# Kernel optimization log

Measured on AMD Instinct MI355X. Metric: run time of the kernel, lower is better.

## Reference

```python
import jax, jax.numpy as jnp
import numpy as np

N, E, B = 250000, 1000000, 500
FD = 78  # num_features_xd


def setup_inputs() -> dict:
    key = jax.random.key(0)
    ks = jax.random.split(key, 24)
    g = lambda i, shape, fan_in: jax.random.normal(ks[i], shape, jnp.float32) / np.sqrt(fan_in)
    inp = {
        "x": jax.random.normal(ks[0], (N, FD), jnp.float32),
        "edge_index": jax.random.randint(ks[1], (2, E), 0, N, jnp.int32),
        "batch": jnp.repeat(jnp.arange(B, dtype=jnp.int32), N // B),  # sorted, every graph non-empty
        "target": jax.random.randint(ks[2], (B, 1000), 0, 26, jnp.int32),
        # GCN layers
        "W1": g(3, (FD, FD), FD), "b1": jnp.zeros((FD,), jnp.float32),
        "W2": g(4, (FD, 2 * FD), FD), "b2": jnp.zeros((2 * FD,), jnp.float32),
        "W3": g(5, (2 * FD, 4 * FD), 2 * FD), "b3": jnp.zeros((4 * FD,), jnp.float32),
        # graph head
        "fcg1_w": g(6, (4 * FD, 1024), 4 * FD), "fcg1_b": jnp.zeros((1024,), jnp.float32),
        "fcg2_w": g(7, (1024, 128), 1024), "fcg2_b": jnp.zeros((128,), jnp.float32),
        # protein branch
        "emb": g(8, (26, 128), 1),
        "conv_w": g(9, (32, 1000, 8), 1000 * 8), "conv_b": jnp.zeros((32,), jnp.float32),
        "fcxt_w": g(10, (32 * 121, 128), 32 * 121), "fcxt_b": jnp.zeros((128,), jnp.float32),
        # fusion head
        "fc1_w": g(11, (256, 1024), 256), "fc1_b": jnp.zeros((1024,), jnp.float32),
        "fc2_w": g(12, (1024, 512), 1024), "fc2_b": jnp.zeros((512,), jnp.float32),
        "out_w": g(13, (512, 1), 512), "out_b": jnp.zeros((1,), jnp.float32),
    }
    return inp


def _gcn_conv(x, W, b, src, dst, dinv, n):
    # PyG GCNConv: out = D^-1/2 (A+I) D^-1/2 (x W) + b, symmetric norm with self-loops
    xw = x @ W
    norm = dinv[src] * dinv[dst]                                   # [E]
    agg = jax.ops.segment_sum(xw[src] * norm[:, None], dst, num_segments=n)
    agg = agg + xw * (dinv * dinv)[:, None]                        # self-loop term
    return agg + b


def reference(x, edge_index, batch, target,
              W1, b1, W2, b2, W3, b3,
              fcg1_w, fcg1_b, fcg2_w, fcg2_b,
              emb, conv_w, conv_b, fcxt_w, fcxt_b,
              fc1_w, fc1_b, fc2_w, fc2_b, out_w, out_b):
    n = x.shape[0]
    src, dst = edge_index[0], edge_index[1]
    # degree with self-loops (edge weights 1)
    deg = jax.ops.segment_sum(jnp.ones((src.shape[0],), x.dtype), dst, num_segments=n) + 1.0
    dinv = jax.lax.rsqrt(deg)

    h = jax.nn.relu(_gcn_conv(x, W1, b1, src, dst, dinv, n))
    h = jax.nn.relu(_gcn_conv(h, W2, b2, src, dst, dinv, n))
    h = jax.nn.relu(_gcn_conv(h, W3, b3, src, dst, dinv, n))

    bsz = fcg2_w.shape[1] * 0 + target.shape[0]  # B
    g = jax.ops.segment_max(h, batch, num_segments=bsz)            # global max pool -> [B, 312]
    g = jax.nn.relu(g @ fcg1_w + fcg1_b)
    g = g @ fcg2_w + fcg2_b                                        # dropout = identity (eval)

    # protein branch: Conv1d over embedding dim (channels = seq positions = 1000)
    e = emb[target]                                                # [B, 1000, 128]
    c = jax.lax.conv_general_dilated(e, conv_w, window_strides=(1,), padding="VALID",
                                     dimension_numbers=("NCH", "OIH", "NCH"))
    c = c + conv_b[None, :, None]                                  # [B, 32, 121]
    xt = c.reshape(bsz, 32 * 121) @ fcxt_w + fcxt_b

    xc = jnp.concatenate([g, xt], axis=1)                          # [B, 256]
    xc = jax.nn.relu(xc @ fc1_w + fc1_b)
    xc = jax.nn.relu(xc @ fc2_w + fc2_b)
    return xc @ out_w + out_b                                      # [B, 1]
```

## Files before the change

### kernel.cpp

```cpp
#include <hip/hip_runtime.h>
#include <hip/hip_bf16.h>

#define DEV_INLINE __device__ __forceinline__

static constexpr int Nn = 250000;
static constexpr int Ee = 1000000;
static constexpr int Bb = 500;
static constexpr int NPB = Nn / Bb;

typedef __attribute__((ext_vector_type(8))) short short8;
typedef __attribute__((ext_vector_type(8))) unsigned short ushort8v;
typedef __attribute__((ext_vector_type(4))) float f32x4;

DEV_INLINE float b2f(__hip_bfloat16 v) { return __bfloat162float(v); }
DEV_INLINE __hip_bfloat16 f2b(float v) { return __float2bfloat16(v); }
DEV_INLINE unsigned short f2bu(float v) {
    __hip_bfloat16 h = __float2bfloat16(v);
    return __builtin_bit_cast(unsigned short, h);
}
DEV_INLINE float bfu2f(unsigned short u) { return __uint_as_float(((unsigned)u) << 16); }

__global__ void k_deg(const int* __restrict__ dst, int* __restrict__ deg) {
    int i = blockIdx.x * 256 + threadIdx.x;
    if (i < Ee) atomicAdd(&deg[dst[i]], 1);
}

__global__ void k_dinv(const int* __restrict__ deg, float* __restrict__ dinv) {
    int i = blockIdx.x * 256 + threadIdx.x;
    if (i < Nn) dinv[i] = rsqrtf((float)deg[i] + 1.0f);
}

__global__ __launch_bounds__(256) void k_scan1(const int* __restrict__ deg,
                                               int* __restrict__ rp,
                                               int* __restrict__ bsum) {
    __shared__ int s[256];
    int t = threadIdx.x;
    int i = blockIdx.x * 256 + t;
    int v = (i < Nn) ? deg[i] : 0;
    s[t] = v;
    __syncthreads();
    for (int off = 1; off < 256; off <<= 1) {
        int x = (t >= off) ? s[t - off] : 0;
        __syncthreads();
        s[t] += x;
        __syncthreads();
    }
    if (i < Nn) rp[i] = s[t] - v;
    if (t == 255) bsum[blockIdx.x] = s[255];
}

__global__ __launch_bounds__(1024) void k_scan2(int* __restrict__ bsum, int nb) {
    __shared__ int s[1024];
    int t = threadIdx.x;
    int v = (t < nb) ? bsum[t] : 0;
    s[t] = v;
    __syncthreads();
    for (int off = 1; off < 1024; off <<= 1) {
        int x = (t >= off) ? s[t - off] : 0;
        __syncthreads();
        s[t] += x;
        __syncthreads();
    }
    if (t < nb) bsum[t] = s[t] - v;
}

__global__ void k_scan3(int* __restrict__ rp, int* __restrict__ cursor,
                        const int* __restrict__ bsum) {
    int i = blockIdx.x * 256 + threadIdx.x;
    if (i < Nn) {
        int v = rp[i] + bsum[blockIdx.x];
        rp[i] = v;
        cursor[i] = v;
    }
    if (i == 0) rp[Nn] = Ee;
}

__global__ void k_scatter(const int* __restrict__ src, const int* __restrict__ dst,
                          const float* __restrict__ dinv, int* __restrict__ cursor,
                          int* __restrict__ col, float* __restrict__ enorm) {
    int i = blockIdx.x * 256 + threadIdx.x;
    if (i >= Ee) return;
    int s = src[i], d = dst[i];
    int pos = atomicAdd(&cursor[d], 1);
    col[pos] = s;
    enorm[pos] = dinv[s] * dinv[d];
}

__global__ void k_xprep(const float* __restrict__ x, unsigned short* __restrict__ xb) {
    int gid = blockIdx.x * 256 + threadIdx.x;
    if (gid >= Nn * 20) return;
    int i = gid / 20;
    int c = gid - 20 * i;
    int k = 4 * c;
    const float* xp = x + (size_t)i * 78;
    ushort4 u;
    u.x = (k + 0 < 78) ? f2bu(xp[k + 0]) : (unsigned short)0;
    u.y = (k + 1 < 78) ? f2bu(xp[k + 1]) : (unsigned short)0;
    u.z = (k + 2 < 78) ? f2bu(xp[k + 2]) : (unsigned short)0;
    u.w = (k + 3 < 78) ? f2bu(xp[k + 3]) : (unsigned short)0;
    *(ushort4*)&xb[(size_t)i * 80 + k] = u;
}

template <int K, int F, int KP, int FP>
__global__ __launch_bounds__(64) void k_wprep(const float* __restrict__ W,
                                              unsigned short* __restrict__ Wb) {
    constexpr int KSTEPS = KP / 32;
    const int nt = blockIdx.x, ks = blockIdx.y;
    const int l = threadIdx.x;
    const int n = nt * 16 + (l & 15);
    unsigned short* o = Wb + ((size_t)(nt * KSTEPS + ks) * 64 + l) * 8;
#pragma unroll
    for (int j = 0; j < 8; ++j) {
        const int k = (l >> 4) * 8 + j + ks * 32;
        o[j] = (k < K && n < F) ? f2bu(W[(size_t)k * F + n]) : (unsigned short)0;
    }
}

template <int KIN, int KP, int F, int FP, int SOUT, bool POOL>
__global__ __launch_bounds__(320) void k_gcn(const __hip_bfloat16* __restrict__ in_,
                                             const int* __restrict__ rp,
                                             const int* __restrict__ col,
                                             const float* __restrict__ enorm,
                                             const float* __restrict__ dinv,
                                             const unsigned short* __restrict__ Wb,
                                             const float* __restrict__ bias,
                                             __hip_bfloat16* __restrict__ out,
                                             float* __restrict__ gpool) {
    constexpr int ROWS = 16, BD = 320, WAVES = 5;
    constexpr int CPR = KIN / 8;
    constexpr int SLOTS = CPR * ROWS;
    constexpr int ECAP = 16 * ROWS;
    constexpr int KSTEPS = KP / 32;
    constexpr int NT = FP / 16;
    constexpr int TPW = NT / WAVES;
    static_assert(KIN % 8 == 0 && KP % 32 == 0 && KP >= KIN && FP % (16 * WAVES) == 0, "pad");
    const unsigned short* in = (const unsigned short*)in_;

    __shared__ alignas(16) unsigned short sh[ROWS * KP];
    __shared__ int sRp[ROWS + 1];
    __shared__ int sCol[ECAP];
    __shared__ float sEn[ECAP];

    const int i0 = blockIdx.x * ROWS;
    const int t = threadIdx.x;

    if (t <= ROWS) sRp[t] = rp[i0 + t];
    const int base = rp[i0];
    const int ne = rp[i0 + ROWS] - base;
    if (ne <= ECAP) {
        for (int e = t; e < ne; e += BD) {
            sCol[e] = col[base + e];
            sEn[e] = enorm[base + e];
        }
    }
    if constexpr (KP > KIN) {
        for (int e = t; e < ROWS * (KP - KIN); e += BD) {
            const int r = e / (KP - KIN);
            sh[r * KP + KIN + (e - r * (KP - KIN))] = 0;
        }
    }
    __syncthreads();

    for (int slot = t; slot < SLOTS; slot += BD) {
        const int r = slot / CPR;
        const int c = slot - r * CPR;
        const int i = i0 + r;
        const size_t coff = (size_t)8 * c;
        const float di = dinv[i];
        const float selfw = di * di;
        float acc[8];
        {
            ushort8v s = *(const ushort8v*)(in + (size_t)i * KIN + coff);
#pragma unroll
            for (int j = 0; j < 8; ++j) acc[j] = bfu2f(s[j]) * selfw;
        }
        const int e0a = sRp[r], e1a = sRp[r + 1];
        if (ne <= ECAP) {
            int j = e0a - base;
            const int jend = e1a - base;
            for (; j + 4 <= jend; j += 4) {
                const int n0 = sCol[j + 0], n1 = sCol[j + 1], n2 = sCol[j + 2], n3 = sCol[j + 3];
                const float w0 = sEn[j + 0], w1 = sEn[j + 1], w2 = sEn[j + 2], w3 = sEn[j + 3];
                ushort8v a0 = *(const ushort8v*)(in + (size_t)n0 * KIN + coff);
                ushort8v a1 = *(const ushort8v*)(in + (size_t)n1 * KIN + coff);
                ushort8v a2 = *(const ushort8v*)(in + (size_t)n2 * KIN + coff);
                ushort8v a3 = *(const ushort8v*)(in + (size_t)n3 * KIN + coff);
#pragma unroll
                for (int q = 0; q < 8; ++q)
                    acc[q] += bfu2f(a0[q]) * w0 + bfu2f(a1[q]) * w1 +
                              bfu2f(a2[q]) * w2 + bfu2f(a3[q]) * w3;
            }
            for (; j < jend; ++j) {
                const int n = sCol[j];
                const float w = sEn[j];
                ushort8v a = *(const ushort8v*)(in + (size_t)n * KIN + coff);
#pragma unroll
                for (int q = 0; q < 8; ++q) acc[q] += bfu2f(a[q]) * w;
            }
        } else {
            for (int j = e0a; j < e1a; ++j) {
                const int n = col[j];
                const float w = enorm[j];
                ushort8v a = *(const ushort8v*)(in + (size_t)n * KIN + coff);
#pragma unroll
                for (int q = 0; q < 8; ++q) acc[q] += bfu2f(a[q]) * w;
            }
        }
        ushort8v o;
#pragma unroll
        for (int q = 0; q < 8; ++q) o[q] = f2bu(acc[q]);
        *(ushort8v*)&sh[r * KP + 8 * c] = o;
    }
    __syncthreads();

    const int w = t >> 6, lane = t & 63;
    const int arow = lane & 15, aquad = lane >> 4;
    short8 afr[KSTEPS];
#pragma unroll
    for (int ks = 0; ks < KSTEPS; ++ks)
        afr[ks] = *(const short8*)&sh[arow * KP + aquad * 8 + ks * 32];

    const bool uni = (i0 / NPB) == ((i0 + ROWS - 1) / NPB);

#pragma unroll
    for (int nti = 0; nti < TPW; ++nti) {
        const int nt = w * TPW + nti;
        const short8* bp = (const short8*)Wb + (size_t)nt * KSTEPS * 64 + lane;
        f32x4 acc = {0.f, 0.f, 0.f, 0.f};
#pragma unroll
        for (int ks = 0; ks < KSTEPS; ++ks) {
            short8 bfr = bp[ks * 64];
            acc = __builtin_amdgcn_mfma_f32_16x16x32_bf16(afr[ks], bfr, acc, 0, 0, 0);
        }
        const int f = nt * 16 + arow;
        const int ib = i0 + aquad * 4;
        if constexpr (!POOL) {
            if (f < F) {
                const float bv = bias[f];
#pragma unroll
                for (int r = 0; r < 4; ++r)
                    out[(size_t)(ib + r) * SOUT + f] = f2b(fmaxf(acc[r] + bv, 0.f));
            } else if (f < SOUT) {
#pragma unroll
                for (int r = 0; r < 4; ++r)
                    out[(size_t)(ib + r) * SOUT + f] = f2b(0.f);
            }
        } else {
            float m = 0.f, v[4];
            const float bv = (f < F) ? bias[f] : 0.f;
#pragma unroll
            for (int r = 0; r < 4; ++r) {
                v[r] = fmaxf(acc[r] + bv, 0.f);
                m = fmaxf(m, v[r]);
            }
            if (uni) {
                m = fmaxf(m, __shfl_xor(m, 16));
                m = fmaxf(m, __shfl_xor(m, 32));
                if (aquad == 0 && f < F)
                    atomicMax((int*)&gpool[(i0 / NPB) * F + f], __float_as_int(m));
            } else if (f < F) {
                const int g0 = ib / NPB, g3 = (ib + 3) / NPB;
                if (g0 == g3) {
                    atomicMax((int*)&gpool[g0 * F + f], __float_as_int(m));
                } else {
#pragma unroll
                    for (int r = 0; r < 4; ++r)
                        atomicMax((int*)&gpool[((ib + r) / NPB) * F + f], __float_as_int(v[r]));
                }
            }
        }
    }
}

template <int K, int FOUT, int KS, bool RELU, int BD>
__global__ __launch_bounds__(BD) void k_fc(const float* __restrict__ in,
                                           const float* __restrict__ W,
                                           const float* __restrict__ bias,
                                           float* __restrict__ out,
                                           int ostride, int ooff) {
    static_assert(!(RELU && KS > 1), "cannot split K with fused ReLU");
    static_assert(K % KS == 0, "K must divide evenly");
    constexpr int KC = K / KS;
    const int j = blockIdx.x * BD + threadIdx.x;
    const int b = blockIdx.y;
    const int z = blockIdx.z;
    const float* __restrict__ inp = in + (size_t)b * K + z * KC;
    const float* __restrict__ Wp = W + (size_t)(z * KC) * FOUT + j;
    float acc = (z == 0) ? bias[j] : 0.f;
#pragma unroll 8
    for (int k = 0; k < KC; ++k) acc += inp[k] * Wp[(size_t)k * FOUT];
    float* dst = &out[(size_t)b * ostride + ooff + j];
    if (KS > 1) {
        atomicAdd(dst, acc);
    } else {
        *dst = RELU ? fmaxf(acc, 0.f) : acc;
    }
}

__global__ __launch_bounds__(128) void k_P(const float* __restrict__ emb,
                                           const float* __restrict__ fcxt_w,
                                           float* __restrict__ P) {
    const int v = blockIdx.x, o = blockIdx.y;
    const int j = threadIdx.x;
    __shared__ float se[128];
    se[j] = emb[v * 128 + j];
    __syncthreads();
    float acc[8];
#pragma unroll
    for (int k = 0; k < 8; ++k) acc[k] = 0.f;
    const float* fw = fcxt_w + (size_t)(o * 121) * 128 + j;
#pragma unroll 4
    for (int h = 0; h < 121; ++h) {
        const float f = fw[(size_t)h * 128];
#pragma unroll
        for (int k = 0; k < 8; ++k) acc[k] += se[h + k] * f;
    }
    float* Pp = P + ((size_t)(v * 32 + o) * 8) * 128 + j;
#pragma unroll
    for (int k = 0; k < 8; ++k) Pp[(size_t)k * 128] = acc[k];
}

__global__ __launch_bounds__(128) void k_T(const float* __restrict__ convw,
                                           const float* __restrict__ P,
                                           float* __restrict__ T) {
    const int i0 = blockIdx.x * 8;
    const int v = blockIdx.y;
    const int t = threadIdx.x;
    __shared__ float wt[8 * 256];
    for (int e = t; e < 2048; e += 128) {
        const int r = e >> 8;
        const int kk = e & 255;
        wt[e] = convw[(size_t)(kk >> 3) * 8000 + (size_t)(i0 + r) * 8 + (kk & 7)];
    }
    __syncthreads();
    float acc[8];
#pragma unroll
    for (int r = 0; r < 8; ++r) acc[r] = 0.f;
    const float* Pp = P + (size_t)v * 256 * 128 + t;
#pragma unroll 2
    for (int kk = 0; kk < 256; ++kk) {
        const float pv = Pp[(size_t)kk * 128];
#pragma unroll
        for (int r = 0; r < 8; ++r) acc[r] += wt[r * 256 + kk] * pv;
    }
    float* Tp = T + ((size_t)v * 1000 + i0) * 128 + t;
#pragma unroll
    for (int r = 0; r < 8; ++r) Tp[(size_t)r * 128] = acc[r];
}

__global__ __launch_bounds__(128) void k_C0(const float* __restrict__ fcxt_w,
                                            const float* __restrict__ fcxt_b,
                                            const float* __restrict__ convb,
                                            float* __restrict__ C0) {
    const int o = blockIdx.x;
    const int j = threadIdx.x;
    float acc = 0.f;
    const float* fw = fcxt_w + (size_t)(o * 121) * 128 + j;
#pragma unroll 4
    for (int h = 0; h < 121; ++h) acc += fw[(size_t)h * 128];
    acc *= convb[o];
    if (o == 0) acc += fcxt_b[j];
    atomicAdd(&C0[j], acc);
}

template <int ZS>
__global__ __launch_bounds__(128) void k_xt(const int* __restrict__ target,
                                            const float* __restrict__ T,
                                            const float* __restrict__ C0,
                                            float* __restrict__ xc) {
    constexpr int CH = 1000 / ZS;
    const int b = blockIdx.x;
    const int z = blockIdx.y;
    const int j = threadIdx.x;
    const int* tg = target + b * 1000 + z * CH;
    float acc = (z == 0) ? C0[j] : 0.f;
    int i = 0;
    for (; i + 4 <= CH; i += 4) {
        const int v0 = tg[i + 0], v1 = tg[i + 1], v2 = tg[i + 2], v3 = tg[i + 3];
        const int ib = z * CH + i;
        acc += T[((size_t)v0 * 1000 + ib + 0) * 128 + j]
             + T[((size_t)v1 * 1000 + ib + 1) * 128 + j]
             + T[((size_t)v2 * 1000 + ib + 2) * 128 + j]
             + T[((size_t)v3 * 1000 + ib + 3) * 128 + j];
    }
    for (; i < CH; ++i) {
        acc += T[((size_t)tg[i] * 1000 + z * CH + i) * 128 + j];
    }
    atomicAdd(&xc[(size_t)b * 256 + 128 + j], acc);
}

__global__ __launch_bounds__(64) void k_out(const float* __restrict__ in,
                                            const float* __restrict__ w,
                                            const float* __restrict__ ob,
                                            float* __restrict__ out) {
    const int b = blockIdx.x;
    const int lane = threadIdx.x;
    const float* p = in + (size_t)b * 512;
    float acc = 0.f;
#pragma unroll
    for (int i = 0; i < 8; ++i) acc += p[lane + 64 * i] * w[lane + 64 * i];
    for (int off = 32; off > 0; off >>= 1) acc += __shfl_down(acc, off);
    if (lane == 0) out[b] = acc + ob[0];
}

extern "C" void kernel_launch(void* const* d_in, const int* in_sizes, int n_in,
                              void* d_out, int out_size, void* d_ws, size_t ws_size,
                              hipStream_t stream) {
    (void)in_sizes; (void)n_in; (void)out_size; (void)ws_size;
    const float* x      = (const float*)d_in[0];
    const int* ei       = (const int*)d_in[1];
    const int* target   = (const int*)d_in[3];
    const float* W1     = (const float*)d_in[4];
    const float* b1     = (const float*)d_in[5];
    const float* W2     = (const float*)d_in[6];
    const float* b2     = (const float*)d_in[7];
    const float* W3     = (const float*)d_in[8];
    const float* b3     = (const float*)d_in[9];
    const float* fcg1_w = (const float*)d_in[10];
    const float* fcg1_b = (const float*)d_in[11];
    const float* fcg2_w = (const float*)d_in[12];
    const float* fcg2_b = (const float*)d_in[13];
    const float* emb    = (const float*)d_in[14];
    const float* conv_w = (const float*)d_in[15];
    const float* conv_b = (const float*)d_in[16];
    const float* fcxt_w = (const float*)d_in[17];
    const float* fcxt_b = (const float*)d_in[18];
    const float* fc1_w  = (const float*)d_in[19];
    const float* fc1_b  = (const float*)d_in[20];
    const float* fc2_w  = (const float*)d_in[21];
    const float* fc2_b  = (const float*)d_in[22];
    const float* out_w  = (const float*)d_in[23];
    const float* out_b  = (const float*)d_in[24];

    const int* src = ei;
    const int* dst = ei + Ee;

    size_t off = 0;
    auto alloc = [&](size_t bytes) -> void* {
        off = (off + 255) & ~(size_t)255;
        void* p = (char*)d_ws + off;
        off += bytes;
        return p;
    };
    int*   deg    = (int*)alloc((size_t)Nn * 4);
    float* dinv   = (float*)alloc((size_t)Nn * 4);
    int*   rp     = (int*)alloc((size_t)(Nn + 1) * 4);
    int*   col    = (int*)alloc((size_t)Ee * 4);
    float* enorm  = (float*)alloc((size_t)Ee * 4);
    int*   bsum   = (int*)alloc(1024 * 4);
    unsigned short* Wb1 = (unsigned short*)alloc((size_t)5 * 3 * 64 * 8 * 2);
    unsigned short* Wb2 = (unsigned short*)alloc((size_t)10 * 3 * 64 * 8 * 2);
    unsigned short* Wb3 = (unsigned short*)alloc((size_t)20 * 5 * 64 * 8 * 2);
    __hip_bfloat16* h1 = (__hip_bfloat16*)alloc((size_t)Nn * 80 * 2);
    __hip_bfloat16* h2 = (__hip_bfloat16*)alloc((size_t)Nn * 160 * 2);
    int* cursor = deg;
    unsigned short* xb = (unsigned short*)h2;

    size_t hoff = 0;
    auto halloc = [&](size_t bytes) -> void* {
        hoff = (hoff + 255) & ~(size_t)255;
        void* p = (char*)h1 + hoff;
        hoff += bytes;
        return p;
    };
    float* gpool = (float*)halloc((size_t)Bb * 312 * 4);
    float* g1    = (float*)halloc((size_t)Bb * 1024 * 4);
    float* xc    = (float*)halloc((size_t)Bb * 256 * 4);
    float* f1    = (float*)halloc((size_t)Bb * 1024 * 4);
    float* f2    = (float*)halloc((size_t)Bb * 512 * 4);
    float* C0    = (float*)halloc(128 * 4);
    float* Pbuf  = (float*)halloc((size_t)26 * 32 * 8 * 128 * 4);
    float* Tbuf  = (float*)halloc((size_t)26 * 1000 * 128 * 4);

    const int nb = (Nn + 255) / 256;

    k_xprep<<<(Nn * 20 + 255) / 256, 256, 0, stream>>>(x, xb);

    hipMemsetAsync(deg, 0, (size_t)Nn * 4, stream);
    k_deg<<<(Ee + 255) / 256, 256, 0, stream>>>(dst, deg);
    k_dinv<<<nb, 256, 0, stream>>>(deg, dinv);
    k_scan1<<<nb, 256, 0, stream>>>(deg, rp, bsum);
    k_scan2<<<1, 1024, 0, stream>>>(bsum, nb);
    k_scan3<<<nb, 256, 0, stream>>>(rp, cursor, bsum);
    k_scatter<<<(Ee + 255) / 256, 256, 0, stream>>>(src, dst, dinv, cursor, col, enorm);

    k_wprep<78, 78, 96, 80><<<dim3(5, 3), 64, 0, stream>>>(W1, Wb1);
    k_wprep<78, 156, 96, 160><<<dim3(10, 3), 64, 0, stream>>>(W2, Wb2);
    k_wprep<156, 312, 160, 320><<<dim3(20, 5), 64, 0, stream>>>(W3, Wb3);

    k_gcn<80, 96, 78, 80, 80, false><<<Nn / 16, 320, 0, stream>>>(
        (const __hip_bfloat16*)xb, rp, col, enorm, dinv, Wb1, b1, h1, (float*)nullptr);
    k_gcn<80, 96, 156, 160, 160, false><<<Nn / 16, 320, 0, stream>>>(
        h1, rp, col, enorm, dinv, Wb2, b2, h2, (float*)nullptr);
    hipMemsetAsync(gpool, 0, (size_t)Bb * 312 * 4, stream);
    k_gcn<160, 160, 312, 320, 0, true><<<Nn / 16, 320, 0, stream>>>(
        h2, rp, col, enorm, dinv, Wb3, b3, (__hip_bfloat16*)nullptr, gpool);

    hipMemsetAsync(C0, 0, 128 * 4, stream);
    hipMemsetAsync(xc, 0, (size_t)Bb * 256 * 4, stream);
    k_P<<<dim3(26, 32), 128, 0, stream>>>(emb, fcxt_w, Pbuf);
    k_T<<<dim3(125, 26), 128, 0, stream>>>(conv_w, Pbuf, Tbuf);
    k_C0<<<32, 128, 0, stream>>>(fcxt_w, fcxt_b, conv_b, C0);
    k_xt<8><<<dim3(Bb, 8), 128, 0, stream>>>(target, Tbuf, C0, xc);

    k_fc<312, 1024, 1, true, 256><<<dim3(4, Bb, 1), 256, 0, stream>>>(gpool, fcg1_w, fcg1_b, g1, 1024, 0);
    k_fc<1024, 128, 2, false, 128><<<dim3(1, Bb, 2), 128, 0, stream>>>(g1, fcg2_w, fcg2_b, xc, 256, 0);

    k_fc<256, 1024, 1, true, 256><<<dim3(4, Bb, 1), 256, 0, stream>>>(xc, fc1_w, fc1_b, f1, 1024, 0);
    k_fc<1024, 512, 1, true, 256><<<dim3(2, Bb, 1), 256, 0, stream>>>(f1, fc2_w, fc2_b, f2, 512, 0);
    k_out<<<Bb, 64, 0, stream>>>(f2, out_w, out_b, (float*)d_out);
}
```

Baseline: 879.2 us.

## Parallelize GCN neighbor aggregation over edges with LDS float atomics

Aggregation in the fused GCN kernel is no longer done by one thread per (row, chunk) looping over that row's neighbors. Work is now split into (edge, chunk) tasks across the whole block, and each task adds into an fp32 shared-memory accumulator with atomicAdd; a per-edge row table is built in LDS. This is meant to remove load imbalance from uneven degrees and expose more memory-level parallelism for the gathers. The cost is LDS atomic traffic, a larger fp32 shared buffer that may reduce occupancy, and a serial per-row fill of the row table.

```diff
diff --git a/kernel.cpp b/kernel.cpp
--- a/kernel.cpp
+++ b/kernel.cpp
@@ -133,13 +133,15 @@
     constexpr int KSTEPS = KP / 32;
     constexpr int NT = FP / 16;
     constexpr int TPW = NT / WAVES;
+    constexpr int KPF = KP + 4;
     static_assert(KIN % 8 == 0 && KP % 32 == 0 && KP >= KIN && FP % (16 * WAVES) == 0, "pad");
     const unsigned short* in = (const unsigned short*)in_;
 
-    __shared__ alignas(16) unsigned short sh[ROWS * KP];
+    __shared__ alignas(16) float accf[ROWS * KPF];
     __shared__ int sRp[ROWS + 1];
     __shared__ int sCol[ECAP];
     __shared__ float sEn[ECAP];
+    __shared__ unsigned char sRow[ECAP];
 
     const int i0 = blockIdx.x * ROWS;
     const int t = threadIdx.x;
@@ -147,69 +149,66 @@
     if (t <= ROWS) sRp[t] = rp[i0 + t];
     const int base = rp[i0];
     const int ne = rp[i0 + ROWS] - base;
-    if (ne <= ECAP) {
+    const bool fit = (ne <= ECAP);
+    if (fit) {
         for (int e = t; e < ne; e += BD) {
             sCol[e] = col[base + e];
             sEn[e] = enorm[base + e];
         }
+        if (t < ROWS) {
+            const int ea = rp[i0 + t] - base, eb = rp[i0 + t + 1] - base;
+            for (int j = ea; j < eb; ++j) sRow[j] = (unsigned char)t;
+        }
     }
     if constexpr (KP > KIN) {
         for (int e = t; e < ROWS * (KP - KIN); e += BD) {
             const int r = e / (KP - KIN);
-            sh[r * KP + KIN + (e - r * (KP - KIN))] = 0;
-        }
-    }
-    __syncthreads();
-
+            accf[r * KPF + KIN + (e - r * (KP - KIN))] = 0.f;
+        }
+    }
     for (int slot = t; slot < SLOTS; slot += BD) {
         const int r = slot / CPR;
         const int c = slot - r * CPR;
         const int i = i0 + r;
-        const size_t coff = (size_t)8 * c;
         const float di = dinv[i];
         const float selfw = di * di;
-        float acc[8];
-        {
-            ushort8v s = *(const ushort8v*)(in + (size_t)i * KIN + coff);
-#pragma unroll
-            for (int j = 0; j < 8; ++j) acc[j] = bfu2f(s[j]) * selfw;
-        }
-        const int e0a = sRp[r], e1a = sRp[r + 1];
-        if (ne <= ECAP) {
-            int j = e0a - base;
-            const int jend = e1a - base;
-            for (; j + 4 <= jend; j += 4) {
-                const int n0 = sCol[j + 0], n1 = sCol[j + 1], n2 = sCol[j + 2], n3 = sCol[j + 3];
-                const float w0 = sEn[j + 0], w1 = sEn[j + 1], w2 = sEn[j + 2], w3 = sEn[j + 3];
-                ushort8v a0 = *(const ushort8v*)(in + (size_t)n0 * KIN + coff);
-                ushort8v a1 = *(const ushort8v*)(in + (size_t)n1 * KIN + coff);
-                ushort8v a2 = *(const ushort8v*)(in + (size_t)n2 * KIN + coff);
-                ushort8v a3 = *(const ushort8v*)(in + (size_t)n3 * KIN + coff);
-#pragma unroll
-                for (int q = 0; q < 8; ++q)
-                    acc[q] += bfu2f(a0[q]) * w0 + bfu2f(a1[q]) * w1 +
-                              bfu2f(a2[q]) * w2 + bfu2f(a3[q]) * w3;
+        ushort8v s = *(const ushort8v*)(in + (size_t)i * KIN + (size_t)8 * c);
+        float* ap = &accf[r * KPF + 8 * c];
+#pragma unroll
+        for (int q = 0; q < 8; ++q) ap[q] = bfu2f(s[q]) * selfw;
+    }
+    __syncthreads();
+
+    const int ntask = ne * CPR;
+    if (fit) {
+        for (int task = t; task < ntask; task += BD) {
+            const int e = task / CPR;
+            const int c = task - e * CPR;
+            const int n = sCol[e];
+            const float w = sEn[e];
+            const int r = sRow[e];
+            ushort8v a = *(const ushort8v*)(in + (size_t)n * KIN + (size_t)8 * c);
+            float* ap = &accf[r * KPF + 8 * c];
+#pragma unroll
+            for (int q = 0; q < 8; ++q) atomicAdd(&ap[q], bfu2f(a[q]) * w);
+        }
+    } else {
+        for (int task = t; task < ntask; task += BD) {
+            const int e = task / CPR;
+            const int c = task - e * CPR;
+            const int n = col[base + e];
+            const float w = enorm[base + e];
+            int lo = 0, hi = ROWS;
+            while (hi - lo > 1) {
+                const int mid = (lo + hi) >> 1;
+                if (sRp[mid] <= base + e) lo = mid; else hi = mid;
             }
-            for (; j < jend; ++j) {
-                const int n = sCol[j];
-                const float w = sEn[j];
-                ushort8v a = *(const ushort8v*)(in + (size_t)n * KIN + coff);
-#pragma unroll
-                for (int q = 0; q < 8; ++q) acc[q] += bfu2f(a[q]) * w;
-            }
-        } else {
-            for (int j = e0a; j < e1a; ++j) {
-                const int n = col[j];
-                const float w = enorm[j];
-                ushort8v a = *(const ushort8v*)(in + (size_t)n * KIN + coff);
-#pragma unroll
-                for (int q = 0; q < 8; ++q) acc[q] += bfu2f(a[q]) * w;
-            }
-        }
-        ushort8v o;
-#pragma unroll
-        for (int q = 0; q < 8; ++q) o[q] = f2bu(acc[q]);
-        *(ushort8v*)&sh[r * KP + 8 * c] = o;
+            const int r = lo;
+            ushort8v a = *(const ushort8v*)(in + (size_t)n * KIN + (size_t)8 * c);
+            float* ap = &accf[r * KPF + 8 * c];
+#pragma unroll
+            for (int q = 0; q < 8; ++q) atomicAdd(&ap[q], bfu2f(a[q]) * w);
+        }
     }
     __syncthreads();
 
@@ -217,8 +216,18 @@
     const int arow = lane & 15, aquad = lane >> 4;
     short8 afr[KSTEPS];
 #pragma unroll
-    for (int ks = 0; ks < KSTEPS; ++ks)
-        afr[ks] = *(const short8*)&sh[arow * KP + aquad * 8 + ks * 32];
+    for (int ks = 0; ks < KSTEPS; ++ks) {
+        const float* ap = &accf[arow * KPF + aquad * 8 + ks * 32];
+        f32x4 lo = *(const f32x4*)ap;
+        f32x4 hi = *(const f32x4*)(ap + 4);
+        short8 fr;
+#pragma unroll
+        for (int q = 0; q < 4; ++q) {
+            fr[q]     = (short)f2bu(lo[q]);
+            fr[4 + q] = (short)f2bu(hi[q]);
+        }
+        afr[ks] = fr;
+    }
 
     const bool uni = (i0 / NPB) == ((i0 + ROWS - 1) / NPB);
 
```

New measurement: 2.278 ms. 159% more time.

## Process 32 rows per block in first GCN layers and use packed FMA

Applied to the files above, without the earlier changes.

The first two GCN layers (KIN=80) now handle 32 rows per 320-thread block, so every thread owns exactly one gather slot where half the threads sat idle before. The MFMA stage loops over 16-row tiles, so each wave reuses the weight fragments across two row tiles. The gather loads the self row before the barrier and accumulates with packed two-wide float FMAs over bf16 pairs, and launch bounds request higher occupancy. In exchange the kernel uses more shared memory for edges and row data, and the occupancy hint may force register spills.

```diff
diff --git a/kernel.cpp b/kernel.cpp
--- a/kernel.cpp
+++ b/kernel.cpp
@@ -10,7 +10,9 @@
 
 typedef __attribute__((ext_vector_type(8))) short short8;
 typedef __attribute__((ext_vector_type(8))) unsigned short ushort8v;
+typedef __attribute__((ext_vector_type(4))) unsigned int uint4v;
 typedef __attribute__((ext_vector_type(4))) float f32x4;
+typedef __attribute__((ext_vector_type(2))) float f32x2;
 
 DEV_INLINE float b2f(__hip_bfloat16 v) { return __bfloat162float(v); }
 DEV_INLINE __hip_bfloat16 f2b(float v) { return __float2bfloat16(v); }
@@ -19,6 +21,20 @@
     return __builtin_bit_cast(unsigned short, h);
 }
 DEV_INLINE float bfu2f(unsigned short u) { return __uint_as_float(((unsigned)u) << 16); }
+
+DEV_INLINE f32x2 pairf(unsigned u) {
+    f32x2 r;
+    r.x = __uint_as_float(u << 16);
+    r.y = __uint_as_float(u & 0xffff0000u);
+    return r;
+}
+DEV_INLINE f32x2 fma2(f32x2 a, f32x2 b, f32x2 c) {
+#if __has_builtin(__builtin_elementwise_fma)
+    return __builtin_elementwise_fma(a, b, c);
+#else
+    return a * b + c;
+#endif
+}
 
 __global__ void k_deg(const int* __restrict__ dst, int* __restrict__ deg) {
     int i = blockIdx.x * 256 + threadIdx.x;
@@ -116,156 +132,180 @@
     }
 }
 
-template <int KIN, int KP, int F, int FP, int SOUT, bool POOL>
-__global__ __launch_bounds__(320) void k_gcn(const __hip_bfloat16* __restrict__ in_,
-                                             const int* __restrict__ rp,
-                                             const int* __restrict__ col,
-                                             const float* __restrict__ enorm,
-                                             const float* __restrict__ dinv,
-                                             const unsigned short* __restrict__ Wb,
-                                             const float* __restrict__ bias,
-                                             __hip_bfloat16* __restrict__ out,
-                                             float* __restrict__ gpool) {
-    constexpr int ROWS = 16, BD = 320, WAVES = 5;
+template <int KIN, int KP, int F, int FP, int SOUT, bool POOL, int MAXROWS>
+__global__ __launch_bounds__(320, 8) void k_gcn(const __hip_bfloat16* __restrict__ in_,
+                                                const int* __restrict__ rp,
+                                                const int* __restrict__ col,
+                                                const float* __restrict__ enorm,
+                                                const float* __restrict__ dinv,
+                                                const unsigned short* __restrict__ Wb,
+                                                const float* __restrict__ bias,
+                                                __hip_bfloat16* __restrict__ out,
+                                                float* __restrict__ gpool) {
+    constexpr int BD = 320, WAVES = 5;
     constexpr int CPR = KIN / 8;
-    constexpr int SLOTS = CPR * ROWS;
-    constexpr int ECAP = 16 * ROWS;
+    constexpr int ECAP = 16 * MAXROWS;
     constexpr int KSTEPS = KP / 32;
     constexpr int NT = FP / 16;
     constexpr int TPW = NT / WAVES;
     static_assert(KIN % 8 == 0 && KP % 32 == 0 && KP >= KIN && FP % (16 * WAVES) == 0, "pad");
+    static_assert(MAXROWS % 16 == 0, "row tiles");
+    static_assert(!POOL || MAXROWS == 16, "pool path assumes 16 rows");
+    static_assert(CPR * MAXROWS == BD, "one slot per thread");
     const unsigned short* in = (const unsigned short*)in_;
 
-    __shared__ alignas(16) unsigned short sh[ROWS * KP];
-    __shared__ int sRp[ROWS + 1];
+    __shared__ alignas(16) unsigned short sh[MAXROWS * KP];
+    __shared__ int sRp[MAXROWS + 1];
     __shared__ int sCol[ECAP];
     __shared__ float sEn[ECAP];
 
-    const int i0 = blockIdx.x * ROWS;
+    const int i0 = blockIdx.x * MAXROWS;
+    const int rows = min(MAXROWS, Nn - i0);
     const int t = threadIdx.x;
-
-    if (t <= ROWS) sRp[t] = rp[i0 + t];
+    const int slots = rows * CPR;
+    const bool act = (t < slots);
+
+    const int r = t / CPR;
+    const int c = t - r * CPR;
+    const size_t coff = (size_t)8 * c;
+    uint4v selfv = {0u, 0u, 0u, 0u};
+    float selfw = 0.f;
+    if (act) {
+        const int i = i0 + r;
+        selfv = *(const uint4v*)(in + (size_t)i * KIN + coff);
+        const float di = dinv[i];
+        selfw = di * di;
+    }
+
+    if (t <= rows) sRp[t] = rp[i0 + t];
     const int base = rp[i0];
-    const int ne = rp[i0 + ROWS] - base;
-    if (ne <= ECAP) {
+    const int ne = rp[i0 + rows] - base;
+    const bool fit = (ne <= ECAP);
+    if (fit) {
         for (int e = t; e < ne; e += BD) {
             sCol[e] = col[base + e];
             sEn[e] = enorm[base + e];
         }
     }
     if constexpr (KP > KIN) {
-        for (int e = t; e < ROWS * (KP - KIN); e += BD) {
-            const int r = e / (KP - KIN);
-            sh[r * KP + KIN + (e - r * (KP - KIN))] = 0;
+        for (int e = t; e < MAXROWS * (KP - KIN); e += BD) {
+            const int rr = e / (KP - KIN);
+            sh[rr * KP + KIN + (e - rr * (KP - KIN))] = 0;
         }
     }
     __syncthreads();
 
-    for (int slot = t; slot < SLOTS; slot += BD) {
-        const int r = slot / CPR;
-        const int c = slot - r * CPR;
-        const int i = i0 + r;
-        const size_t coff = (size_t)8 * c;
-        const float di = dinv[i];
-        const float selfw = di * di;
-        float acc[8];
-        {
-            ushort8v s = *(const ushort8v*)(in + (size_t)i * KIN + coff);
-#pragma unroll
-            for (int j = 0; j < 8; ++j) acc[j] = bfu2f(s[j]) * selfw;
-        }
+    if (act) {
+        f32x2 acc2[4];
+#pragma unroll
+        for (int q = 0; q < 4; ++q) acc2[q] = pairf(selfv[q]) * selfw;
+
         const int e0a = sRp[r], e1a = sRp[r + 1];
-        if (ne <= ECAP) {
+        if (fit) {
             int j = e0a - base;
             const int jend = e1a - base;
             for (; j + 4 <= jend; j += 4) {
                 const int n0 = sCol[j + 0], n1 = sCol[j + 1], n2 = sCol[j + 2], n3 = sCol[j + 3];
                 const float w0 = sEn[j + 0], w1 = sEn[j + 1], w2 = sEn[j + 2], w3 = sEn[j + 3];
-                ushort8v a0 = *(const ushort8v*)(in + (size_t)n0 * KIN + coff);
-                ushort8v a1 = *(const ushort8v*)(in + (size_t)n1 * KIN + coff);
-                ushort8v a2 = *(const ushort8v*)(in + (size_t)n2 * KIN + coff);
-                ushort8v a3 = *(const ushort8v*)(in + (size_t)n3 * KIN + coff);
-#pragma unroll
-                for (int q = 0; q < 8; ++q)
-                    acc[q] += bfu2f(a0[q]) * w0 + bfu2f(a1[q]) * w1 +
-                              bfu2f(a2[q]) * w2 + bfu2f(a3[q]) * w3;
+                uint4v a0 = *(const uint4v*)(in + (size_t)n0 * KIN + coff);
+                uint4v a1 = *(const uint4v*)(in + (size_t)n1 * KIN + coff);
+                uint4v a2 = *(const uint4v*)(in + (size_t)n2 * KIN + coff);
+                uint4v a3 = *(const uint4v*)(in + (size_t)n3 * KIN + coff);
+                const f32x2 w0v = {w0, w0}, w1v = {w1, w1}, w2v = {w2, w2}, w3v = {w3, w3};
+#pragma unroll
+                for (int q = 0; q < 4; ++q) {
+                    acc2[q] = fma2(pairf(a0[q]), w0v, acc2[q]);
+                    acc2[q] = fma2(pairf(a1[q]), w1v, acc2[q]);
+                    acc2[q] = fma2(pairf(a2[q]), w2v, acc2[q]);
+                    acc2[q] = fma2(pairf(a3[q]), w3v, acc2[q]);
+                }
             }
             for (; j < jend; ++j) {
                 const int n = sCol[j];
-                const float w = sEn[j];
-                ushort8v a = *(const ushort8v*)(in + (size_t)n * KIN + coff);
-#pragma unroll
-                for (int q = 0; q < 8; ++q) acc[q] += bfu2f(a[q]) * w;
+                const float wv = sEn[j];
+                const f32x2 wvv = {wv, wv};
+                uint4v a = *(const uint4v*)(in + (size_t)n * KIN + coff);
+#pragma unroll
+                for (int q = 0; q < 4; ++q) acc2[q] = fma2(pairf(a[q]), wvv, acc2[q]);
             }
         } else {
             for (int j = e0a; j < e1a; ++j) {
                 const int n = col[j];
-                const float w = enorm[j];
-                ushort8v a = *(const ushort8v*)(in + (size_t)n * KIN + coff);
-#pragma unroll
-                for (int q = 0; q < 8; ++q) acc[q] += bfu2f(a[q]) * w;
+                const float wv = enorm[j];
+                const f32x2 wvv = {wv, wv};
+                uint4v a = *(const uint4v*)(in + (size_t)n * KIN + coff);
+#pragma unroll
+                for (int q = 0; q < 4; ++q) acc2[q] = fma2(pairf(a[q]), wvv, acc2[q]);
             }
         }
         ushort8v o;
 #pragma unroll
-        for (int q = 0; q < 8; ++q) o[q] = f2bu(acc[q]);
+        for (int q = 0; q < 4; ++q) {
+            o[2 * q + 0] = f2bu(acc2[q].x);
+            o[2 * q + 1] = f2bu(acc2[q].y);
+        }
         *(ushort8v*)&sh[r * KP + 8 * c] = o;
     }
     __syncthreads();
 
     const int w = t >> 6, lane = t & 63;
     const int arow = lane & 15, aquad = lane >> 4;
-    short8 afr[KSTEPS];
-#pragma unroll
-    for (int ks = 0; ks < KSTEPS; ++ks)
-        afr[ks] = *(const short8*)&sh[arow * KP + aquad * 8 + ks * 32];
-
-    const bool uni = (i0 / NPB) == ((i0 + ROWS - 1) / NPB);
-
-#pragma unroll
-    for (int nti = 0; nti < TPW; ++nti) {
-        const int nt = w * TPW + nti;
-        const short8* bp = (const short8*)Wb + (size_t)nt * KSTEPS * 64 + lane;
-        f32x4 acc = {0.f, 0.f, 0.f, 0.f};
-#pragma unroll
-        for (int ks = 0; ks < KSTEPS; ++ks) {
-            short8 bfr = bp[ks * 64];
-            acc = __builtin_amdgcn_mfma_f32_16x16x32_bf16(afr[ks], bfr, acc, 0, 0, 0);
-        }
-        const int f = nt * 16 + arow;
-        const int ib = i0 + aquad * 4;
-        if constexpr (!POOL) {
-            if (f < F) {
-                const float bv = bias[f];
-#pragma unroll
-                for (int r = 0; r < 4; ++r)
-                    out[(size_t)(ib + r) * SOUT + f] = f2b(fmaxf(acc[r] + bv, 0.f));
-            } else if (f < SOUT) {
-#pragma unroll
-                for (int r = 0; r < 4; ++r)
-                    out[(size_t)(ib + r) * SOUT + f] = f2b(0.f);
+    const int nrt = rows >> 4;
+
+    for (int rt = 0; rt < nrt; ++rt) {
+        short8 afr[KSTEPS];
+#pragma unroll
+        for (int ks = 0; ks < KSTEPS; ++ks)
+            afr[ks] = *(const short8*)&sh[(rt * 16 + arow) * KP + aquad * 8 + ks * 32];
+
+        const int ir0 = i0 + rt * 16;
+        const bool uni = (ir0 / NPB) == ((ir0 + 15) / NPB);
+
+#pragma unroll
+        for (int nti = 0; nti < TPW; ++nti) {
+            const int nt = w * TPW + nti;
+            const short8* bp = (const short8*)Wb + (size_t)nt * KSTEPS * 64 + lane;
+            f32x4 acc = {0.f, 0.f, 0.f, 0.f};
+#pragma unroll
+            for (int ks = 0; ks < KSTEPS; ++ks) {
+                short8 bfr = bp[ks * 64];
+                acc = __builtin_amdgcn_mfma_f32_16x16x32_bf16(afr[ks], bfr, acc, 0, 0, 0);
             }
-        } else {
-            float m = 0.f, v[4];
-            const float bv = (f < F) ? bias[f] : 0.f;
-#pragma unroll
-            for (int r = 0; r < 4; ++r) {
-                v[r] = fmaxf(acc[r] + bv, 0.f);
-                m = fmaxf(m, v[r]);
-            }
-            if (uni) {
-                m = fmaxf(m, __shfl_xor(m, 16));
-                m = fmaxf(m, __shfl_xor(m, 32));
-                if (aquad == 0 && f < F)
-                    atomicMax((int*)&gpool[(i0 / NPB) * F + f], __float_as_int(m));
-            } else if (f < F) {
-                const int g0 = ib / NPB, g3 = (ib + 3) / NPB;
-                if (g0 == g3) {
-                    atomicMax((int*)&gpool[g0 * F + f], __float_as_int(m));
-                } else {
-#pragma unroll
-                    for (int r = 0; r < 4; ++r)
-                        atomicMax((int*)&gpool[((ib + r) / NPB) * F + f], __float_as_int(v[r]));
+            const int f = nt * 16 + arow;
+            const int ib = ir0 + aquad * 4;
+            if constexpr (!POOL) {
+                if (f < F) {
+                    const float bv = bias[f];
+#pragma unroll
+                    for (int rr = 0; rr < 4; ++rr)
+                        out[(size_t)(ib + rr) * SOUT + f] = f2b(fmaxf(acc[rr] + bv, 0.f));
+                } else if (f < SOUT) {
+#pragma unroll
+                    for (int rr = 0; rr < 4; ++rr)
+                        out[(size_t)(ib + rr) * SOUT + f] = f2b(0.f);
+                }
+            } else {
+                float m = 0.f, v[4];
+                const float bv = (f < F) ? bias[f] : 0.f;
+#pragma unroll
+                for (int rr = 0; rr < 4; ++rr) {
+                    v[rr] = fmaxf(acc[rr] + bv, 0.f);
+                    m = fmaxf(m, v[rr]);
+                }
+                if (uni) {
+                    m = fmaxf(m, __shfl_xor(m, 16));
+                    m = fmaxf(m, __shfl_xor(m, 32));
+                    if (aquad == 0 && f < F)
+                        atomicMax((int*)&gpool[(ir0 / NPB) * F + f], __float_as_int(m));
+                } else if (f < F) {
+                    const int g0 = ib / NPB, g3 = (ib + 3) / NPB;
+                    if (g0 == g3) {
+                        atomicMax((int*)&gpool[g0 * F + f], __float_as_int(m));
+                    } else {
+#pragma unroll
+                        for (int rr = 0; rr < 4; ++rr)
+                            atomicMax((int*)&gpool[((ib + rr) / NPB) * F + f], __float_as_int(v[rr]));
+                    }
                 }
             }
         }
@@ -488,12 +528,13 @@
     k_wprep<78, 156, 96, 160><<<dim3(10, 3), 64, 0, stream>>>(W2, Wb2);
     k_wprep<156, 312, 160, 320><<<dim3(20, 5), 64, 0, stream>>>(W3, Wb3);
 
-    k_gcn<80, 96, 78, 80, 80, false><<<Nn / 16, 320, 0, stream>>>(
+    const int g32 = (Nn + 31) / 32;
+    k_gcn<80, 96, 78, 80, 80, false, 32><<<g32, 320, 0, stream>>>(
         (const __hip_bfloat16*)xb, rp, col, enorm, dinv, Wb1, b1, h1, (float*)nullptr);
-    k_gcn<80, 96, 156, 160, 160, false><<<Nn / 16, 320, 0, stream>>>(
+    k_gcn<80, 96, 156, 160, 160, false, 32><<<g32, 320, 0, stream>>>(
         h1, rp, col, enorm, dinv, Wb2, b2, h2, (float*)nullptr);
     hipMemsetAsync(gpool, 0, (size_t)Bb * 312 * 4, stream);
-    k_gcn<160, 160, 312, 320, 0, true><<<Nn / 16, 320, 0, stream>>>(
+    k_gcn<160, 160, 312, 320, 0, true, 16><<<Nn / 16, 320, 0, stream>>>(
         h2, rp, col, enorm, dinv, Wb3, b3, (__hip_bfloat16*)nullptr, gpool);
 
     hipMemsetAsync(C0, 0, 128 * 4, stream);
```

Result: faster. 844.2 us (-4.0%).
